# Kernel optimization log

Hardware: AMD Instinct MI355X
Metric: run time of the kernel (lower is better)

Reference implementation:

```python
import jax, jax.numpy as jnp
import numpy as np


def setup_inputs() -> dict:
    key = jax.random.key(0)
    k1, k2 = jax.random.split(key)
    B, S, F, C = 4, 1024, 512, 4   # batch, time, freq bins, in_filters
    T, K, O = 2, 4, 4              # time half-window, harmonics, out_filters
    x_in = jax.random.normal(k1, (B, S, F, C), dtype=jnp.float32)
    W = jax.random.normal(k2, (2 * T + 1, K, C, O), dtype=jnp.float32) * 0.05
    return {"x_in": x_in, "W": W}


def reference(x_in, W):
    # W: [2T+1, K, C, O]
    T = (W.shape[0] - 1) // 2
    K = W.shape[1]
    B, S, F, C = x_in.shape
    # pad time axis by T on each side (as in tf.pad in the original)
    x_pad = jnp.pad(x_in, ((0, 0), (T, T), (0, 0), (0, 0)))  # [B, S+2T, F, C]
    # harmonic index table: idx[omega, k] = (k+1) * omega, masked when out of band
    k_range = jnp.arange(1, K + 1)                 # [K]
    omega = jnp.arange(F)                          # [F]
    idx = omega[:, None] * k_range[None, :]        # [F, K]
    valid = (idx < F)                              # [F, K]
    idx_c = jnp.clip(idx, 0, F - 1)
    # vectorized harmonic gather over all (time, freq): [B, S+2T, F, K, C]
    xh = x_pad[:, :, idx_c, :] * valid[None, None, :, :, None].astype(x_pad.dtype)
    # windowed time combination: small fixed loop over 2T+1 taps avoids
    # materializing the [B, S, 2T+1, F, K, C] patch tensor
    out = jnp.zeros((B, S, F, W.shape[-1]), dtype=x_in.dtype)
    for t in range(2 * T + 1):
        out = out + jnp.einsum('bsfkc,kco->bsfo', xh[:, t:t + S], W[t])
    return out
```

## Files before the change

kernel.cpp:

```cpp
#include <hip/hip_runtime.h>


#define TS    4
#define NTAP  5
#define FB    512
#define SB    1024
#define BB    4

__global__ __launch_bounds__(256, 4)
void harmonic_conv_kernel(const float* __restrict__ x,
                          const float* __restrict__ W,
                          float* __restrict__ out) {
    const int bid  = blockIdx.x;
    const int work = ((bid & 7) << 7) + (bid >> 3);
    const int b    = work >> 8;
    const int s0   = (work & 255) * TS;
    const int tid  = threadIdx.x;

    const float4* xb = (const float4*)x + (size_t)b * SB * FB;
    float4*       ob = (float4*)out + (size_t)b * SB * FB;

    {
        const int g = tid + 256;
        float4 xw[TS + 4];
#pragma unroll
        for (int r = 0; r < TS + 4; ++r) {
            const int sp = s0 + r - 2;
            xw[r] = (sp >= 0 && sp < SB) ? xb[(size_t)sp * FB + g]
                                         : make_float4(0.f, 0.f, 0.f, 0.f);
        }
        float4 acc[TS];
#pragma unroll
        for (int j = 0; j < TS; ++j) acc[j] = make_float4(0.f, 0.f, 0.f, 0.f);
#pragma unroll
        for (int t = 0; t < NTAP; ++t) {
            const float* wp = W + t * 64;
            float w[16];
#pragma unroll
            for (int i = 0; i < 16; ++i) w[i] = wp[i];
#pragma unroll
            for (int j = 0; j < TS; ++j) {
                const float4 xv = xw[j + t];
                acc[j].x += xv.x*w[0] + xv.y*w[4] + xv.z*w[8]  + xv.w*w[12];
                acc[j].y += xv.x*w[1] + xv.y*w[5] + xv.z*w[9]  + xv.w*w[13];
                acc[j].z += xv.x*w[2] + xv.y*w[6] + xv.z*w[10] + xv.w*w[14];
                acc[j].w += xv.x*w[3] + xv.y*w[7] + xv.z*w[11] + xv.w*w[15];
            }
        }
#pragma unroll
        for (int j = 0; j < TS; ++j)
            ob[(size_t)(s0 + j) * FB + g] = acc[j];
    }

    {
        const int f = tid;
        float4 acc[TS];
#pragma unroll
        for (int j = 0; j < TS; ++j) acc[j] = make_float4(0.f, 0.f, 0.f, 0.f);

#pragma unroll
        for (int m = 1; m <= 4; ++m) {
            const int g = f * m;
            if (g < FB) {
                float4 xw[TS + 4];
#pragma unroll
                for (int r = 0; r < TS + 4; ++r) {
                    const int sp = s0 + r - 2;
                    xw[r] = (sp >= 0 && sp < SB) ? xb[(size_t)sp * FB + g]
                                                 : make_float4(0.f, 0.f, 0.f, 0.f);
                }
#pragma unroll
                for (int t = 0; t < NTAP; ++t) {
                    const float* wp = W + t * 64 + (m - 1) * 16;
                    float w[16];
#pragma unroll
                    for (int i = 0; i < 16; ++i) w[i] = wp[i];
#pragma unroll
                    for (int j = 0; j < TS; ++j) {
                        const float4 xv = xw[j + t];
                        acc[j].x += xv.x*w[0] + xv.y*w[4] + xv.z*w[8]  + xv.w*w[12];
                        acc[j].y += xv.x*w[1] + xv.y*w[5] + xv.z*w[9]  + xv.w*w[13];
                        acc[j].z += xv.x*w[2] + xv.y*w[6] + xv.z*w[10] + xv.w*w[14];
                        acc[j].w += xv.x*w[3] + xv.y*w[7] + xv.z*w[11] + xv.w*w[15];
                    }
                }
            }
        }
#pragma unroll
        for (int j = 0; j < TS; ++j)
            ob[(size_t)(s0 + j) * FB + f] = acc[j];
    }
}

extern "C" void kernel_launch(void* const* d_in, const int* in_sizes, int n_in,
                              void* d_out, int out_size, void* d_ws, size_t ws_size,
                              hipStream_t stream) {
    const float* x = (const float*)d_in[0];
    const float* W = (const float*)d_in[1];
    float* out = (float*)d_out;
    const int nblocks = BB * (SB / TS);
    harmonic_conv_kernel<<<nblocks, 256, 0, stream>>>(x, W, out);
}
```

Baseline: 95.09 us.

## Stage time rows in LDS ring buffer with swizzle and prefetch harmonics

Each block now handles 8 time steps and keeps a rolling window of input rows in shared memory, arranged as an 8-slot ring buffer with an XOR swizzle. Harmonic gathers read from LDS instead of global memory, and the next two rows are prefetched into registers while the current step computes. This is meant to cut redundant global and L2 reads for strided harmonic gathers and overlapping time windows. In exchange it adds 64KB of LDS per block, one barrier per step, and only 512 blocks with lower occupancy.

New measurement: 93.46 us. Within noise of the previous version (-1.7%).

```diff
diff --git a/kernel.cpp b/kernel.cpp
--- a/kernel.cpp
+++ b/kernel.cpp
@@ -1,94 +1,112 @@
 #include <hip/hip_runtime.h>
 
 
-#define TS    4
+#define SC    8
+#define NSLOT 8
 #define NTAP  5
 #define FB    512
 #define SB    1024
 #define BB    4
+#define ROWP  512
 
-__global__ __launch_bounds__(256, 4)
+__device__ __forceinline__ int swz(int f) { return f ^ ((f >> 4) & 7); }
+
+__device__ __forceinline__ void accum_harm(const float4* lx, const int* slotbase,
+                                           int g, const float* __restrict__ Wk,
+                                           float4 acc[2]) {
+    float4 xw[6];
+#pragma unroll
+    for (int r = 0; r < 6; ++r) xw[r] = lx[slotbase[r] + swz(g)];
+#pragma unroll
+    for (int t = 0; t < NTAP; ++t) {
+        const float* wp = Wk + t * 64;
+        float w[16];
+#pragma unroll
+        for (int i = 0; i < 16; ++i) w[i] = wp[i];
+#pragma unroll
+        for (int j = 0; j < 2; ++j) {
+            const float4 xv = xw[j + t];
+            acc[j].x += xv.x*w[0] + xv.y*w[4] + xv.z*w[8]  + xv.w*w[12];
+            acc[j].y += xv.x*w[1] + xv.y*w[5] + xv.z*w[9]  + xv.w*w[13];
+            acc[j].z += xv.x*w[2] + xv.y*w[6] + xv.z*w[10] + xv.w*w[14];
+            acc[j].w += xv.x*w[3] + xv.y*w[7] + xv.z*w[11] + xv.w*w[15];
+        }
+    }
+}
+
+__global__ __launch_bounds__(256, 2)
 void harmonic_conv_kernel(const float* __restrict__ x,
                           const float* __restrict__ W,
                           float* __restrict__ out) {
-    const int bid  = blockIdx.x;
-    const int work = ((bid & 7) << 7) + (bid >> 3);
-    const int b    = work >> 8;
-    const int s0   = (work & 255) * TS;
-    const int tid  = threadIdx.x;
+    __shared__ float4 lx[NSLOT * ROWP];
+
+    const int bid = blockIdx.x;
+    const int b   = bid >> 7;
+    const int c   = (bid & 127) * SC;
+    const int tid = threadIdx.x;
 
     const float4* xb = (const float4*)x + (size_t)b * SB * FB;
     float4*       ob = (float4*)out + (size_t)b * SB * FB;
 
-    {
-        const int g = tid + 256;
-        float4 xw[TS + 4];
 #pragma unroll
-        for (int r = 0; r < TS + 4; ++r) {
-            const int sp = s0 + r - 2;
-            xw[r] = (sp >= 0 && sp < SB) ? xb[(size_t)sp * FB + g]
-                                         : make_float4(0.f, 0.f, 0.f, 0.f);
+    for (int r = 0; r < 6; ++r) {
+        const int sp = c - 2 + r;
+#pragma unroll
+        for (int h = 0; h < 2; ++h) {
+            const int col = h * 256 + tid;
+            float4 v = make_float4(0.f, 0.f, 0.f, 0.f);
+            if (sp >= 0 && sp < SB) v = xb[(size_t)sp * FB + col];
+            lx[r * ROWP + swz(col)] = v;
         }
-        float4 acc[TS];
+    }
+    __syncthreads();
+
+#pragma unroll 1
+    for (int st = 0; st < SC; st += 2) {
+        float4 sv[4];
+        const bool do_stage = (st < SC - 2);
+        if (do_stage) {
+            const int r0 = c + st + 4, r1 = c + st + 5;
 #pragma unroll
-        for (int j = 0; j < TS; ++j) acc[j] = make_float4(0.f, 0.f, 0.f, 0.f);
-#pragma unroll
-        for (int t = 0; t < NTAP; ++t) {
-            const float* wp = W + t * 64;
-            float w[16];
-#pragma unroll
-            for (int i = 0; i < 16; ++i) w[i] = wp[i];
-#pragma unroll
-            for (int j = 0; j < TS; ++j) {
-                const float4 xv = xw[j + t];
-                acc[j].x += xv.x*w[0] + xv.y*w[4] + xv.z*w[8]  + xv.w*w[12];
-                acc[j].y += xv.x*w[1] + xv.y*w[5] + xv.z*w[9]  + xv.w*w[13];
-                acc[j].z += xv.x*w[2] + xv.y*w[6] + xv.z*w[10] + xv.w*w[14];
-                acc[j].w += xv.x*w[3] + xv.y*w[7] + xv.z*w[11] + xv.w*w[15];
+            for (int h = 0; h < 2; ++h) {
+                sv[h]     = (r0 < SB) ? xb[(size_t)r0 * FB + h * 256 + tid]
+                                      : make_float4(0.f, 0.f, 0.f, 0.f);
+                sv[2 + h] = (r1 < SB) ? xb[(size_t)r1 * FB + h * 256 + tid]
+                                      : make_float4(0.f, 0.f, 0.f, 0.f);
             }
         }
+
+        int slotbase[6];
 #pragma unroll
-        for (int j = 0; j < TS; ++j)
-            ob[(size_t)(s0 + j) * FB + g] = acc[j];
-    }
+        for (int r = 0; r < 6; ++r) slotbase[r] = ((st + r) & 7) * ROWP;
 
-    {
-        const int f = tid;
-        float4 acc[TS];
+        float4 acc[2];
+
+        acc[0] = make_float4(0.f, 0.f, 0.f, 0.f);
+        acc[1] = make_float4(0.f, 0.f, 0.f, 0.f);
+        accum_harm(lx, slotbase, tid + 256, W, acc);
 #pragma unroll
-        for (int j = 0; j < TS; ++j) acc[j] = make_float4(0.f, 0.f, 0.f, 0.f);
+        for (int j = 0; j < 2; ++j)
+            ob[(size_t)(c + st + j) * FB + (tid + 256)] = acc[j];
 
+        acc[0] = make_float4(0.f, 0.f, 0.f, 0.f);
+        acc[1] = make_float4(0.f, 0.f, 0.f, 0.f);
+        accum_harm(lx, slotbase, tid,     W,      acc);
+        accum_harm(lx, slotbase, tid * 2, W + 16, acc);
+        if (tid * 3 < FB) accum_harm(lx, slotbase, tid * 3, W + 32, acc);
+        if (tid * 4 < FB) accum_harm(lx, slotbase, tid * 4, W + 48, acc);
 #pragma unroll
-        for (int m = 1; m <= 4; ++m) {
-            const int g = f * m;
-            if (g < FB) {
-                float4 xw[TS + 4];
+        for (int j = 0; j < 2; ++j)
+            ob[(size_t)(c + st + j) * FB + tid] = acc[j];
+
+        if (do_stage) {
 #pragma unroll
-                for (int r = 0; r < TS + 4; ++r) {
-                    const int sp = s0 + r - 2;
-                    xw[r] = (sp >= 0 && sp < SB) ? xb[(size_t)sp * FB + g]
-                                                 : make_float4(0.f, 0.f, 0.f, 0.f);
-                }
-#pragma unroll
-                for (int t = 0; t < NTAP; ++t) {
-                    const float* wp = W + t * 64 + (m - 1) * 16;
-                    float w[16];
-#pragma unroll
-                    for (int i = 0; i < 16; ++i) w[i] = wp[i];
-#pragma unroll
-                    for (int j = 0; j < TS; ++j) {
-                        const float4 xv = xw[j + t];
-                        acc[j].x += xv.x*w[0] + xv.y*w[4] + xv.z*w[8]  + xv.w*w[12];
-                        acc[j].y += xv.x*w[1] + xv.y*w[5] + xv.z*w[9]  + xv.w*w[13];
-                        acc[j].z += xv.x*w[2] + xv.y*w[6] + xv.z*w[10] + xv.w*w[14];
-                        acc[j].w += xv.x*w[3] + xv.y*w[7] + xv.z*w[11] + xv.w*w[15];
-                    }
-                }
+            for (int h = 0; h < 2; ++h) {
+                lx[((st + 6) & 7) * ROWP + swz(h * 256 + tid)] = sv[h];
+                lx[((st + 7) & 7) * ROWP + swz(h * 256 + tid)] = sv[2 + h];
             }
         }
-#pragma unroll
-        for (int j = 0; j < TS; ++j)
-            ob[(size_t)(s0 + j) * FB + f] = acc[j];
+        __syncthreads();
     }
 }
 
@@ -98,6 +116,6 @@
     const float* x = (const float*)d_in[0];
     const float* W = (const float*)d_in[1];
     float* out = (float*)d_out;
-    const int nblocks = BB * (SB / TS);
+    const int nblocks = BB * (SB / SC);
     harmonic_conv_kernel<<<nblocks, 256, 0, stream>>>(x, W, out);
 }
```
